# Optimization experiments

Measured on AMD Instinct MI355X. Metric: run time of the kernel, lower is better.

Reference implementation:

```python
import jax, jax.numpy as jnp
import numpy as np

T, B, D = 128, 2048, 256
ALPHA = 0.5
VTH = 1.0


def _gl_coeffs(n):
    # c[0]=1; c[j] = (1 - (1+alpha)/j) * c[j-1], computed in float64 then cast
    j = np.arange(1, n + 1, dtype=np.float64)
    c = np.concatenate([[1.0], np.cumprod(1.0 - (1.0 + ALPHA) / j)])
    return jnp.asarray(c, dtype=jnp.float32)  # [n+1]


def lorentz_expmap(z, v, eps=1e-6):
    # Minkowski inner product <v,v>_L = -v0^2 + ||v_1:||^2 (curvature -1 hyperboloid)
    vv = -v[..., 0] ** 2 + jnp.sum(v[..., 1:] ** 2, axis=-1)
    s = jnp.sqrt(jnp.clip(vv, eps, None))[..., None]  # [B,1]
    return jnp.cosh(s) * z + (jnp.sinh(s) / s) * v


def setup_inputs() -> dict:
    key = jax.random.key(0)
    k1, k2, k3 = jax.random.split(key, 3)
    x_seq = jax.random.normal(k1, (T, B, D), dtype=jnp.float32)
    # point on the hyperboloid: z = [sqrt(1+||zs||^2), zs]
    zs = 0.1 * jax.random.normal(k2, (B, D - 1), dtype=jnp.float32)
    z0 = jnp.sqrt(1.0 + jnp.sum(zs ** 2, axis=-1, keepdims=True))
    z_seq = jnp.concatenate([z0, zs], axis=-1)  # [B, D]
    # tangent vector at z: <z,v>_L = 0  =>  v0 = <zs, vs>/z0
    vs = 0.1 * jax.random.normal(k3, (B, D - 1), dtype=jnp.float32)
    v0 = jnp.sum(zs * vs, axis=-1, keepdims=True) / z0
    v_seq = jnp.concatenate([v0, vs], axis=-1)  # [B, D]
    return {"x_seq": x_seq, "v_seq": v_seq, "z_seq": z_seq}


def _gl_if_scan(x_seq):
    n = x_seq.shape[0]
    c = _gl_coeffs(n)  # [n+1]
    idx = jnp.arange(n)  # buffer slot i holds y[i+1]; y[0] = 0 always

    def step(Y, inp):
        x_k, k = inp  # k in 1..n
        # right = sum_{j=1..k} c[j] * y[k-j]; y[0]=0 so only slots i < k-1 contribute,
        # with weight c[k-1-i] for buffer slot i (holding y[i+1])
        w = jnp.where(idx < k - 1, c[jnp.clip(k - 1 - idx, 0, n)], 0.0)  # [n]
        right = jnp.tensordot(w, Y, axes=1)  # [B, D]
        men = x_k - right  # h^alpha = 1 since h = 1
        spike = (men > VTH).astype(x_k.dtype)
        men = men - VTH * spike
        Y = jax.lax.dynamic_update_slice(Y, men[None], (k - 1, 0, 0))
        return Y, spike

    Y0 = jnp.zeros_like(x_seq)  # [n, B, D] history of reset membrane potentials
    ks = jnp.arange(1, n + 1)
    _, s_seq = jax.lax.scan(step, Y0, (x_seq, ks))
    return s_seq  # [n, B, D]


def reference(x_seq, v_seq, z_seq):
    s_seq = _gl_if_scan(x_seq)
    z_out = lorentz_expmap(z_seq, v_seq)
    return (s_seq, z_out)
```

## Files before the change

kernel.cpp:

```cpp
#include <hip/hip_runtime.h>
#include <math.h>

#define TT 128
#define BB 2048
#define DDIM 256
#define BD (BB * DDIM)

struct Coeffs {
    float c[TT + 1];
};
static constexpr Coeffs make_coeffs() {
    Coeffs r{};
    r.c[0] = 1.0f;
    double cur = 1.0;
    for (int j = 1; j <= TT; ++j) {
        cur *= (1.0 - 1.5 / (double)j);
        r.c[j] = (float)cur;
    }
    return r;
}
static constexpr Coeffs CO = make_coeffs();

__global__ __launch_bounds__(256) void gl_if_kernel(const float* __restrict__ x,
                                                    float* __restrict__ sp) {
    const int g = blockIdx.x * 256 + threadIdx.x;
    float y[TT];

#pragma unroll
    for (int k = 1; k <= TT; ++k) {
        const float xk = x[(size_t)(k - 1) * BD + g];
        float acc = 0.0f;
#pragma unroll
        for (int i = 0; i <= k - 2; ++i) {
            acc = fmaf(CO.c[k - 1 - i], y[i], acc);
        }
        const float men0 = xk - acc;
        const float spike = (men0 > 1.0f) ? 1.0f : 0.0f;
        y[k - 1] = men0 - spike;
        sp[(size_t)(k - 1) * BD + g] = spike;
    }
}

__global__ __launch_bounds__(256) void expmap_kernel(const float* __restrict__ v,
                                                     const float* __restrict__ z,
                                                     float* __restrict__ out) {
    const int b = blockIdx.x;
    const int d = threadIdx.x;
    const size_t idx = (size_t)b * DDIM + d;
    const float vd = v[idx];

    float term = vd * vd;
    if (d == 0) term = -term;

    float sum = term;
#pragma unroll
    for (int off = 32; off > 0; off >>= 1) sum += __shfl_down(sum, off, 64);

    __shared__ float ws[4];
    if ((threadIdx.x & 63) == 0) ws[threadIdx.x >> 6] = sum;
    __syncthreads();
    const float vv = ws[0] + ws[1] + ws[2] + ws[3];

    const float s2 = fmaxf(vv, 1e-6f);
    const float s = sqrtf(s2);
    const float ch = coshf(s);
    const float shs = sinhf(s) / s;

    out[idx] = ch * z[idx] + shs * vd;
}

extern "C" void kernel_launch(void* const* d_in, const int* in_sizes, int n_in,
                              void* d_out, int out_size, void* d_ws, size_t ws_size,
                              hipStream_t stream) {
    const float* x_seq = (const float*)d_in[0];
    const float* v_seq = (const float*)d_in[1];
    const float* z_seq = (const float*)d_in[2];

    float* s_out = (float*)d_out;
    float* z_out = (float*)d_out + (size_t)TT * BD;

    gl_if_kernel<<<BD / 256, 256, 0, stream>>>(x_seq, s_out);
    expmap_kernel<<<BB, DDIM, 0, stream>>>(v_seq, z_seq, z_out);
}
```

Measured before the change: 135.3 us.

## Load GL coefficients from global memory, prefetch inputs, and limit occupancy with LDS ballast

A tiny kernel now writes the Grünwald-Letnikov coefficients into the workspace once, and the scan kernel reads them through uniform global loads instead of embedding them as compile-time constants. A 48KB shared-memory array that is otherwise unused caps the number of blocks per CU, likely to ease pressure on the 128-entry register history or the cache. The input x is also software-prefetched two steps ahead. These changes add an extra kernel launch and many scalar coefficient loads per step, and they deliberately reduce occupancy, so latency hiding depends on fewer waves.

```diff
diff --git a/kernel.cpp b/kernel.cpp
--- a/kernel.cpp
+++ b/kernel.cpp
@@ -6,38 +6,50 @@
 #define DDIM 256
 #define BD (BB * DDIM)
 
-struct Coeffs {
-    float c[TT + 1];
-};
-static constexpr Coeffs make_coeffs() {
-    Coeffs r{};
-    r.c[0] = 1.0f;
-    double cur = 1.0;
-    for (int j = 1; j <= TT; ++j) {
-        cur *= (1.0 - 1.5 / (double)j);
-        r.c[j] = (float)cur;
+__global__ void coeff_init_kernel(float* __restrict__ c) {
+    if (blockIdx.x == 0 && threadIdx.x == 0) {
+        c[0] = 1.0f;
+        double cur = 1.0;
+        for (int j = 1; j < TT; ++j) {
+            cur *= (1.0 - 1.5 / (double)j);
+            c[j] = (float)cur;
+        }
     }
-    return r;
 }
-static constexpr Coeffs CO = make_coeffs();
 
 __global__ __launch_bounds__(256) void gl_if_kernel(const float* __restrict__ x,
-                                                    float* __restrict__ sp) {
+                                                    float* __restrict__ sp,
+                                                    const float* __restrict__ C) {
+    __shared__ float lds_ballast[12288];
+
     const int g = blockIdx.x * 256 + threadIdx.x;
+
+    lds_ballast[threadIdx.x] = x[g];
+    float keep = lds_ballast[(threadIdx.x + 7) & 255];
+    asm volatile("" ::"v"(keep));
+
     float y[TT];
+
+    float xa = x[g];
+    float xb = x[g + BD];
 
 #pragma unroll
     for (int k = 1; k <= TT; ++k) {
-        const float xk = x[(size_t)(k - 1) * BD + g];
+        float xc = 0.0f;
+        if (k + 2 <= TT) {
+            xc = x[g + (size_t)(k + 1) * BD];
+        }
         float acc = 0.0f;
 #pragma unroll
         for (int i = 0; i <= k - 2; ++i) {
-            acc = fmaf(CO.c[k - 1 - i], y[i], acc);
+            acc = fmaf(C[k - 1 - i], y[i], acc);
         }
-        const float men0 = xk - acc;
+        const float men0 = xa - acc;
         const float spike = (men0 > 1.0f) ? 1.0f : 0.0f;
         y[k - 1] = men0 - spike;
-        sp[(size_t)(k - 1) * BD + g] = spike;
+        sp[g + (size_t)(k - 1) * BD] = spike;
+        xa = xb;
+        xb = xc;
     }
 }
 
@@ -78,7 +90,9 @@
 
     float* s_out = (float*)d_out;
     float* z_out = (float*)d_out + (size_t)TT * BD;
+    float* coeffs = (float*)d_ws;
 
-    gl_if_kernel<<<BD / 256, 256, 0, stream>>>(x_seq, s_out);
+    coeff_init_kernel<<<1, 64, 0, stream>>>(coeffs);
+    gl_if_kernel<<<BD / 256, 256, 0, stream>>>(x_seq, s_out, coeffs);
     expmap_kernel<<<BB, DDIM, 0, stream>>>(v_seq, z_seq, z_out);
 }
```

Result: slower. 285.8 us (+111.3%).

## Block GL recurrence into 16-step chunks with batched loads

Applied to the files above, without the earlier changes.

Restructures the per-thread fractional-memory recurrence into chunks of 16 time steps. It loads 16 inputs at once so memory latency overlaps, then accumulates the history contribution for each chunk as a 16x16 block of independent FMAs before running the causal in-chunk solve. This is meant to expose more memory-level and instruction-level parallelism than the serial per-step loop. An empty asm barrier pins the history values in registers, which risks higher register pressure and a different FMA summation order.

```diff
diff --git a/kernel.cpp b/kernel.cpp
--- a/kernel.cpp
+++ b/kernel.cpp
@@ -27,17 +27,49 @@
     float y[TT];
 
 #pragma unroll
-    for (int k = 1; k <= TT; ++k) {
-        const float xk = x[(size_t)(k - 1) * BD + g];
-        float acc = 0.0f;
+    for (int K = 0; K < TT / 16; ++K) {
+        float xv[16];
 #pragma unroll
-        for (int i = 0; i <= k - 2; ++i) {
-            acc = fmaf(CO.c[k - 1 - i], y[i], acc);
+        for (int r = 0; r < 16; ++r) {
+            xv[r] = x[g + (size_t)(16 * K + r) * BD];
         }
-        const float men0 = xk - acc;
-        const float spike = (men0 > 1.0f) ? 1.0f : 0.0f;
-        y[k - 1] = men0 - spike;
-        sp[(size_t)(k - 1) * BD + g] = spike;
+
+        float acc[16];
+#pragma unroll
+        for (int r = 0; r < 16; ++r) acc[r] = 0.0f;
+
+#pragma unroll
+        for (int I = 0; I < K; ++I) {
+            float yt[16];
+#pragma unroll
+            for (int s = 0; s < 16; ++s) {
+                yt[s] = y[16 * I + s];
+                asm("" : "+v"(yt[s]));
+            }
+#pragma unroll
+            for (int r = 0; r < 16; ++r) {
+#pragma unroll
+                for (int s = 0; s < 16; ++s) {
+                    acc[r] = fmaf(CO.c[16 * (K - I) + r - s], yt[s], acc[r]);
+                }
+            }
+        }
+
+        float yn[16];
+#pragma unroll
+        for (int r = 0; r < 16; ++r) {
+            float a = acc[r];
+#pragma unroll
+            for (int s = 0; s < 16; ++s) {
+                if (s <= r - 1) a = fmaf(CO.c[r - s], yn[s], a);
+            }
+            const float men0 = xv[r] - a;
+            const float spike = (men0 > 1.0f) ? 1.0f : 0.0f;
+            yn[r] = men0 - spike;
+            sp[g + (size_t)(16 * K + r) * BD] = spike;
+        }
+#pragma unroll
+        for (int r = 0; r < 16; ++r) y[16 * K + r] = yn[r];
     }
 }
 
```

Result: slower. 246.5 us (+82.2%).
